# Optimization experiments

Hardware: AMD Instinct MI355X
Metric: run time of the kernel (lower is better)

The kernel has to match this reference:

```python
import math
import jax, jax.numpy as jnp
import numpy as np

N_HEADS = 8
GROUPS = 32
EPS = 1e-5


def setup_inputs() -> dict:
    key = jax.random.key(0)
    ks = jax.random.split(key, 4)
    B, C, H, W = 8, 512, 32, 32
    x = jax.random.normal(ks[0], (B, C, H, W), dtype=jnp.float32)
    gn_scale = jnp.ones((C,), dtype=jnp.float32)
    gn_bias = jnp.zeros((C,), dtype=jnp.float32)
    # small init so softmax logits stay in a sane range (original zero-inits
    # proj_out; we use small random weights so the output is non-trivial)
    qkv_w = jax.random.normal(ks[1], (3 * C, C), dtype=jnp.float32) * 0.02
    qkv_b = jnp.zeros((3 * C,), dtype=jnp.float32)
    proj_w = jax.random.normal(ks[2], (C, C), dtype=jnp.float32) * 0.02
    proj_b = jnp.zeros((C,), dtype=jnp.float32)
    return {"x": x, "gn_scale": gn_scale, "gn_bias": gn_bias,
            "qkv_w": qkv_w, "qkv_b": qkv_b,
            "proj_w": proj_w, "proj_b": proj_b}


def reference(x, gn_scale, gn_bias, qkv_w, qkv_b, proj_w, proj_b):
    b, c, H, W = x.shape
    L = H * W
    xr = x.reshape(b, c, L)

    # GroupNorm32: normalize in fp32 over (channels_per_group, L)
    xf = xr.astype(jnp.float32).reshape(b, GROUPS, -1)
    mu = xf.mean(axis=-1, keepdims=True)
    var = xf.var(axis=-1, keepdims=True)
    xn = ((xf - mu) * jax.lax.rsqrt(var + EPS)).reshape(b, c, L)
    xn = (xn * gn_scale[:, None] + gn_bias[:, None]).astype(x.dtype)

    # 1x1 conv QKV projection: [b, 3C, L]
    qkv = jnp.einsum('oc,bcl->bol', qkv_w, xn) + qkv_b[:, None]

    # QKVAttentionLegacy: split 3C axis as (heads, 3*ch)
    ch = c // N_HEADS
    qkv = qkv.reshape(b * N_HEADS, 3 * ch, L)
    q, k, v = qkv[:, :ch], qkv[:, ch:2 * ch], qkv[:, 2 * ch:]
    scale = 1.0 / math.sqrt(math.sqrt(ch))
    w = jnp.einsum('bct,bcs->bts', q * scale, k * scale)  # [b*h, L, L]
    w = jax.nn.softmax(w.astype(jnp.float32), axis=-1).astype(qkv.dtype)
    a = jnp.einsum('bts,bcs->bct', w, v).reshape(b, c, L)

    # 1x1 conv output projection + residual
    h = jnp.einsum('oc,bcl->bol', proj_w, a) + proj_b[:, None]
    return (xr + h).reshape(b, c, H, W)
```

## Files before the change

### kernel.cpp

```cpp
#include <hip/hip_runtime.h>
#include <hip/hip_bf16.h>

typedef __attribute__((ext_vector_type(8))) short v8s;
typedef __attribute__((ext_vector_type(4))) short v4s;
typedef __attribute__((ext_vector_type(8))) unsigned short u16x8;
typedef __attribute__((ext_vector_type(4))) float v4f;

#define MFMA16(a, b, c) __builtin_amdgcn_mfma_f32_16x16x32_bf16((a), (b), (c), 0, 0, 0)

#if __has_builtin(__builtin_amdgcn_mfma_f32_16x16x16_bf16)
#define MFMA16K16(a, b, c) __builtin_amdgcn_mfma_f32_16x16x16_bf16((a), (b), (c), 0, 0, 0)
#elif __has_builtin(__builtin_amdgcn_mfma_f32_16x16x16bf16_1k)
#define MFMA16K16(a, b, c) __builtin_amdgcn_mfma_f32_16x16x16bf16_1k((a), (b), (c), 0, 0, 0)
#else
static __device__ __forceinline__ v4f mfma16k16_asm(v4s a, v4s b, v4f c) {
  v4f d;
  asm("v_mfma_f32_16x16x16_bf16 %0, %1, %2, %3" : "=v"(d) : "v"(a), "v"(b), "v"(c));
  return d;
}
#define MFMA16K16(a, b, c) mfma16k16_asm((a), (b), (c))
#endif

#define GLL16(g, l)                                                        \
  __builtin_amdgcn_global_load_lds(                                        \
      (const __attribute__((address_space(1))) unsigned int*)(g),          \
      (__attribute__((address_space(3))) unsigned int*)(l), 16, 0, 0)

#if __has_builtin(__builtin_amdgcn_exp2f)
__device__ __forceinline__ float exp2n(float x) { return __builtin_amdgcn_exp2f(x); }
#else
__device__ __forceinline__ float exp2n(float x) {
  float r; asm("v_exp_f32 %0, %1" : "=v"(r) : "v"(x)); return r;
}
#endif

__device__ __forceinline__ unsigned short f2bf(float f) {
  union { float f; unsigned u; } v; v.f = f;
  unsigned r = v.u + 0x7fffu + ((v.u >> 16) & 1u);
  return (unsigned short)(r >> 16);
}
__device__ __forceinline__ unsigned packbf2(float lo, float hi) {
  union { float f; unsigned u; } a, b; a.f = lo; b.f = hi;
  return (a.u >> 16) | (b.u & 0xffff0000u);
}

__global__ __launch_bounds__(256) void cvt_gn_kernel(const float* __restrict__ in0,
                                                     unsigned short* __restrict__ out0,
                                                     const float* __restrict__ in1,
                                                     unsigned short* __restrict__ out1,
                                                     int n0, int n1,
                                                     const float* __restrict__ x,
                                                     float2* __restrict__ stats) {
  if (blockIdx.x < 1024) {
    int i = blockIdx.x * 256 + threadIdx.x;
    const float* in; unsigned short* out;
    if (i < n0) { in = in0; out = out0; }
    else        { i -= n0; if (i >= n1) return; in = in1; out = out1; }
    float4 v = ((const float4*)in)[i];
    ushort4 o;
    o.x = f2bf(v.x); o.y = f2bf(v.y); o.z = f2bf(v.z); o.w = f2bf(v.w);
    ((ushort4*)out)[i] = o;
    return;
  }
  const int bg = blockIdx.x - 1024;
  const float4* xp4 = (const float4*)(x + (size_t)bg * 16 * 1024);
  float s = 0.f, ss = 0.f;
  for (int i = threadIdx.x; i < 4096; i += 256) {
    float4 v = xp4[i];
    s  += (v.x + v.y) + (v.z + v.w);
    ss += (v.x * v.x + v.y * v.y) + (v.z * v.z + v.w * v.w);
  }
  #pragma unroll
  for (int d = 1; d < 64; d <<= 1) { s += __shfl_xor(s, d); ss += __shfl_xor(ss, d); }
  __shared__ float red[2][4];
  const int w = threadIdx.x >> 6;
  if ((threadIdx.x & 63) == 0) { red[0][w] = s; red[1][w] = ss; }
  __syncthreads();
  if (threadIdx.x == 0) {
    s  = red[0][0] + red[0][1] + red[0][2] + red[0][3];
    ss = red[1][0] + red[1][1] + red[1][2] + red[1][3];
    const float mu  = s * (1.f / 16384.f);
    const float var = ss * (1.f / 16384.f) - mu * mu;
    stats[bg] = make_float2(mu, rsqrtf(var + 1e-5f));
  }
}

__global__ __launch_bounds__(256) void gnt_kernel(const float* __restrict__ x,
                                                  const float2* __restrict__ stats,
                                                  const float* __restrict__ gsc,
                                                  const float* __restrict__ gbi,
                                                  unsigned short* __restrict__ xnT) {
  const int b = blockIdx.z, l0 = blockIdx.x * 64, c0 = blockIdx.y * 64;
  const float* sp = x + (size_t)b * 512 * 1024;
  unsigned short* dp = xnT + (size_t)b * 1024 * 512;
  __shared__ unsigned T[64][65];
  const int tid = threadIdx.x;
  const int rr = tid >> 3, c8 = (tid & 7) * 8;
  #pragma unroll
  for (int sw = 0; sw < 2; ++sw) {
    const int c = c0 + sw * 32 + rr;
    const float2 st = stats[b * 32 + (c >> 4)];
    const float sc = gsc[c] * st.y;
    const float bi = gbi[c] - st.x * sc;
    const float4* px = (const float4*)(sp + (size_t)c * 1024 + l0 + c8);
    float4 v0 = px[0], v1 = px[1];
    T[sw * 32 + rr][c8 + 0] = f2bf(v0.x * sc + bi);
    T[sw * 32 + rr][c8 + 1] = f2bf(v0.y * sc + bi);
    T[sw * 32 + rr][c8 + 2] = f2bf(v0.z * sc + bi);
    T[sw * 32 + rr][c8 + 3] = f2bf(v0.w * sc + bi);
    T[sw * 32 + rr][c8 + 4] = f2bf(v1.x * sc + bi);
    T[sw * 32 + rr][c8 + 5] = f2bf(v1.y * sc + bi);
    T[sw * 32 + rr][c8 + 6] = f2bf(v1.z * sc + bi);
    T[sw * 32 + rr][c8 + 7] = f2bf(v1.w * sc + bi);
  }
  __syncthreads();
  #pragma unroll
  for (int sw = 0; sw < 2; ++sw) {
    const int ll = sw * 32 + rr;
    u16x8 o;
    #pragma unroll
    for (int j = 0; j < 8; ++j) o[j] = (unsigned short)T[c8 + j][ll];
    *(u16x8*)(dp + (size_t)(l0 + ll) * 512 + c0 + c8) = o;
  }
}

template <bool QKV, int NT>
__global__ __launch_bounds__(256) void gemm_kernel(
    const unsigned short* __restrict__ A,
    const unsigned short* __restrict__ BT,
    const float* __restrict__ bias,
    const float* __restrict__ xres,
    float* __restrict__ outf,
    unsigned short* __restrict__ qT,
    unsigned short* __restrict__ kT,
    unsigned short* __restrict__ vO) {
  constexpr int K = 512;
  constexpr int NFR = NT / 32;
  constexpr int NJOB = 16 + NT / 8;
  const int n0 = blockIdx.x * NT, m0 = blockIdx.y * 128, b = blockIdx.z;
  const unsigned short* Bp = BT + (size_t)b * 1024 * K;

  __shared__ __align__(16) unsigned short As[128][64];
  __shared__ __align__(16) unsigned short Bs[NT][64];

  const int tid = threadIdx.x, lane = tid & 63, w = tid >> 6;
  const int quad = lane >> 4, l15 = lane & 15;
  const int wm = (w >> 1) * 64, wn = (w & 1) * (NT / 2);
  const int srow = lane >> 3;
  const int scol = ((lane & 7) ^ srow) * 8;
  const int ck0 = ((quad ^ (l15 & 7)) * 8);
  const int ck1 = ck0 ^ 32;
  const unsigned short* Asf = &As[0][0];
  const unsigned short* Bsf = &Bs[0][0];

  v4f acc[4][NFR];
  #pragma unroll
  for (int i = 0; i < 4; ++i)
    #pragma unroll
    for (int j = 0; j < NFR; ++j) acc[i][j] = (v4f){0.f, 0.f, 0.f, 0.f};

  for (int kk = 0; kk < K; kk += 64) {
    __syncthreads();
    #pragma unroll
    for (int jj = 0; jj < NJOB / 4; ++jj) {
      const int job = w * (NJOB / 4) + jj;
      if (job < 16) {
        GLL16(A + (size_t)(m0 + job * 8 + srow) * K + kk + scol, &As[job * 8][0]);
      } else {
        const int j2 = job - 16;
        GLL16(Bp + (size_t)(n0 + j2 * 8 + srow) * K + kk + scol, &Bs[j2 * 8][0]);
      }
    }
    __syncthreads();
    #pragma unroll
    for (int h = 0; h < 2; ++h) {
      const int ck = h ? ck1 : ck0;
      v8s af[4], bf[NFR];
      #pragma unroll
      for (int mt = 0; mt < 4; ++mt) af[mt] = *(const v8s*)(Asf + (wm + mt * 16 + l15) * 64 + ck);
      #pragma unroll
      for (int nt = 0; nt < NFR; ++nt) bf[nt] = *(const v8s*)(Bsf + (wn + nt * 16 + l15) * 64 + ck);
      #pragma unroll
      for (int mt = 0; mt < 4; ++mt)
        #pragma unroll
        for (int nt = 0; nt < NFR; ++nt)
          acc[mt][nt] = MFMA16(af[mt], bf[nt], acc[mt][nt]);
    }
  }

  if (QKV) {
    const int bh8 = b * 8;
    const float cs = 0.18033688011112042f;
    #pragma unroll
    for (int mt = 0; mt < 4; ++mt) {
      const int m4 = m0 + wm + mt * 16 + quad * 4;
      const int h = m4 / 192;
      const int rr = m4 - h * 192;
      const int part = rr >> 6;
      const int ch = rr & 63;
      const float b0 = bias[m4], b1 = bias[m4 + 1], b2 = bias[m4 + 2], b3 = bias[m4 + 3];
      #pragma unroll
      for (int nt = 0; nt < NFR; ++nt) {
        const int n = n0 + wn + nt * 16 + l15;
        v4f a = acc[mt][nt];
        const float v0 = a[0] + b0, v1 = a[1] + b1, v2 = a[2] + b2, v3 = a[3] + b3;
        if (part == 0) {
          ushort4 st4;
          st4.x = f2bf(v0 * cs); st4.y = f2bf(v1 * cs);
          st4.z = f2bf(v2 * cs); st4.w = f2bf(v3 * cs);
          *(ushort4*)(qT + ((size_t)(bh8 + h) * 1024 + n) * 64 + ch) = st4;
        } else if (part == 1) {
          ushort4 st4;
          st4.x = f2bf(v0); st4.y = f2bf(v1); st4.z = f2bf(v2); st4.w = f2bf(v3);
          *(ushort4*)(kT + ((size_t)(bh8 + h) * 1024 + n) * 64 + ch) = st4;
        } else {
          unsigned short* dp = vO + ((size_t)(bh8 + h) * 64 + ch) * 1024 + n;
          dp[0] = f2bf(v0); dp[1024] = f2bf(v1); dp[2048] = f2bf(v2); dp[3072] = f2bf(v3);
        }
      }
    }
  } else {
    #pragma unroll
    for (int mt = 0; mt < 4; ++mt) {
      const int m4 = m0 + wm + mt * 16 + quad * 4;
      const float b0 = bias[m4], b1 = bias[m4 + 1], b2 = bias[m4 + 2], b3 = bias[m4 + 3];
      #pragma unroll
      for (int nt = 0; nt < NFR; ++nt) {
        const int n = n0 + wn + nt * 16 + l15;
        const size_t i0 = ((size_t)b * 512 + m4) * 1024 + n;
        outf[i0]        = xres[i0]        + acc[mt][nt][0] + b0;
        outf[i0 + 1024] = xres[i0 + 1024] + acc[mt][nt][1] + b1;
        outf[i0 + 2048] = xres[i0 + 2048] + acc[mt][nt][2] + b2;
        outf[i0 + 3072] = xres[i0 + 3072] + acc[mt][nt][3] + b3;
      }
    }
  }
}

__global__ __launch_bounds__(256) void attn_kernel(const unsigned short* __restrict__ qT,
                                                   const unsigned short* __restrict__ kT,
                                                   const unsigned short* __restrict__ vv,
                                                   unsigned short* __restrict__ aT) {
  const int bh = blockIdx.x;
  const int t0 = blockIdx.y * 256;
  const unsigned short* qb = qT + (size_t)bh * 1024 * 64;
  const unsigned short* kb = kT + (size_t)bh * 1024 * 64;
  const unsigned short* vb = vv + (size_t)bh * 64 * 1024;

  __shared__ __align__(16) unsigned short Ks[2][128][64];
  __shared__ __align__(16) unsigned short Vs[2][2][64][64];

  const int tid = threadIdx.x, w = tid >> 6, lane = tid & 63;
  const int quad = lane >> 4, l15 = lane & 15;
  const int srow = lane >> 3;
  const int scol = ((lane & 7) ^ srow) * 8;
  const int ck0 = ((quad ^ (l15 & 7)) * 8);
  const int ck1 = ck0 ^ 32;

  #pragma unroll
  for (int jj = 0; jj < 8; ++jj) {
    const int seg = w * 8 + jj;
    GLL16(qb + (size_t)(t0 + seg * 8 + srow) * 64 + scol, &Ks[0][0][0] + seg * 8 * 64);
  }
  __syncthreads();
  v8s qf[4][2];
  #pragma unroll
  for (int tg = 0; tg < 4; ++tg) {
    const int row = w * 64 + tg * 16 + l15;
    qf[tg][0] = *(const v8s*)(&Ks[0][0][0] + row * 64 + ck0);
    qf[tg][1] = *(const v8s*)(&Ks[0][0][0] + row * 64 + ck1);
  }
  __syncthreads();

  #pragma unroll
  for (int jj = 0; jj < 8; ++jj) {
    const int j = w * 8 + jj;
    if (j < 16) {
      GLL16(kb + (size_t)(j * 8 + srow) * 64 + scol, &Ks[0][j * 8][0]);
    } else {
      const int j2 = j - 16, hf = j2 >> 3, cg = (j2 & 7) * 8;
      GLL16(vb + (size_t)(cg + srow) * 1024 + hf * 64 + scol, &Vs[0][hf][cg][0]);
    }
  }

  v4f o[4][4];
  #pragma unroll
  for (int tg = 0; tg < 4; ++tg)
    #pragma unroll
    for (int i = 0; i < 4; ++i) o[tg][i] = (v4f){0.f, 0.f, 0.f, 0.f};
  float lsum[4] = {0.f, 0.f, 0.f, 0.f};

  const int vq4 = (quad & 1) * 4;
  const int vqh = quad >> 1;

  for (int it = 0; it < 8; ++it) {
    __syncthreads();
    if (it + 1 < 8) {
      const int s1 = (it + 1) * 128, bp1 = (it + 1) & 1;
      #pragma unroll
      for (int jj = 0; jj < 8; ++jj) {
        const int j = w * 8 + jj;
        if (j < 16) {
          GLL16(kb + (size_t)(s1 + j * 8 + srow) * 64 + scol, &Ks[bp1][j * 8][0]);
        } else {
          const int j2 = j - 16, hf = j2 >> 3, cg = (j2 & 7) * 8;
          GLL16(vb + (size_t)(cg + srow) * 1024 + s1 + hf * 64 + scol,
                &Vs[bp1][hf][cg][0]);
        }
      }
    }
    const int buf = it & 1;

    #pragma unroll
    for (int hf = 0; hf < 2; ++hf) {
      const unsigned short* Kb = &Ks[buf][hf * 64][0];
      const unsigned short* Vb = &Vs[buf][hf][0][0];

      v8s kf[4][2];
      #pragma unroll
      for (int st = 0; st < 4; ++st) {
        kf[st][0] = *(const v8s*)(Kb + (st * 16 + l15) * 64 + ck0);
        kf[st][1] = *(const v8s*)(Kb + (st * 16 + l15) * 64 + ck1);
      }
      v4s vfr[4][4];
      #pragma unroll
      for (int nc = 0; nc < 4; ++nc) {
        const int row = nc * 16 + l15;
        const unsigned short* vrow = Vb + row * 64 + vq4;
        const int rx = row & 7;
        #pragma unroll
        for (int st = 0; st < 4; ++st)
          vfr[nc][st] = *(const v4s*)(vrow + ((st * 2 + vqh) ^ rx) * 8);
      }

      #pragma unroll
      for (int tg = 0; tg < 4; ++tg) {
        v4f sa[4];
        #pragma unroll
        for (int st = 0; st < 4; ++st) {
          v4f z = (v4f){0.f, 0.f, 0.f, 0.f};
          z = MFMA16(kf[st][0], qf[tg][0], z);
          sa[st] = MFMA16(kf[st][1], qf[tg][1], z);
        }
        union { v4s v; unsigned u[2]; } pa[4];
        float rsum = 0.f;
        #pragma unroll
        for (int st = 0; st < 4; ++st) {
          float p0 = exp2n(sa[st][0]);
          float p1 = exp2n(sa[st][1]);
          float p2 = exp2n(sa[st][2]);
          float p3 = exp2n(sa[st][3]);
          rsum += (p0 + p1) + (p2 + p3);
          pa[st].u[0] = packbf2(p0, p1);
          pa[st].u[1] = packbf2(p2, p3);
        }
        lsum[tg] += rsum;
        #pragma unroll
        for (int nc = 0; nc < 4; ++nc)
          #pragma unroll
          for (int st = 0; st < 4; ++st)
            o[tg][nc] = MFMA16K16(pa[st].v, vfr[nc][st], o[tg][nc]);
      }
    }
  }

  const int b = bh >> 3, h = bh & 7;
  #pragma unroll
  for (int tg = 0; tg < 4; ++tg) {
    lsum[tg] += __shfl_xor(lsum[tg], 16);
    lsum[tg] += __shfl_xor(lsum[tg], 32);
  }
  #pragma unroll
  for (int tg = 0; tg < 4; ++tg) {
    float rl[4];
    #pragma unroll
    for (int r = 0; r < 4; ++r) rl[r] = 1.0f / __shfl(lsum[tg], quad * 4 + r);
    #pragma unroll
    for (int nc = 0; nc < 4; ++nc)
      #pragma unroll
      for (int r = 0; r < 4; ++r) {
        aT[((size_t)b * 1024 + t0 + w * 64 + tg * 16 + quad * 4 + r) * 512 +
           h * 64 + nc * 16 + l15] = f2bf(o[tg][nc][r] * rl[r]);
      }
  }
}

extern "C" void kernel_launch(void* const* d_in, const int* in_sizes, int n_in,
                              void* d_out, int out_size, void* d_ws, size_t ws_size,
                              hipStream_t stream) {
  const float* x    = (const float*)d_in[0];
  const float* gsc  = (const float*)d_in[1];
  const float* gbi  = (const float*)d_in[2];
  const float* qkvw = (const float*)d_in[3];
  const float* qkvb = (const float*)d_in[4];
  const float* pjw  = (const float*)d_in[5];
  const float* pjb  = (const float*)d_in[6];
  float* out = (float*)d_out;

  unsigned short* ws  = (unsigned short*)d_ws;
  unsigned short* qw  = ws;
  unsigned short* pw  = qw + 786432;
  float2* stats = (float2*)(pw + 262144);
  unsigned short* xnT = pw + 262144 + 1024;
  unsigned short* qT  = xnT + 4194304;
  unsigned short* kT  = qT + 4194304;
  unsigned short* vv  = kT + 4194304;
  unsigned short* aT  = vv + 4194304;

  cvt_gn_kernel<<<dim3(1280), dim3(256), 0, stream>>>(qkvw, qw, pjw, pw, 196608, 65536,
                                                      x, stats);
  gnt_kernel<<<dim3(16, 8, 8), dim3(256), 0, stream>>>(x, stats, gsc, gbi, xnT);
  gemm_kernel<true, 128><<<dim3(8, 12, 8), dim3(256), 0, stream>>>(
      qw, xnT, qkvb, nullptr, nullptr, qT, kT, vv);
  attn_kernel<<<dim3(64, 4), dim3(256), 0, stream>>>(qT, kT, vv, aT);
  gemm_kernel<false, 64><<<dim3(16, 4, 8), dim3(256), 0, stream>>>(
      pw, aT, pjb, x, out, nullptr, nullptr, nullptr);
}
```

Measured before the change: 149.4 us.

## Switch attention kernel to 32x32x16 MFMA with permlane-based P repacking

Rewrites the attention inner loop to use 32x32x16 bf16 MFMA tiles for both QK^T and PV instead of 16x16 tiles. The softmax probabilities are packed with v_cvt_pk_bf16_f32 and rearranged between lane halves using v_permlane32_swap so they can feed the PV MFMA directly. This is meant to cut MFMA issue count and LDS fragment loads per flop. In exchange it uses larger accumulators, which raises register pressure, and it relies on gfx950-specific instructions. The packing also changes rounding of P from truncation to the hardware conversion.

```diff
diff --git a/kernel.cpp b/kernel.cpp
--- a/kernel.cpp
+++ b/kernel.cpp
@@ -2,24 +2,12 @@
 #include <hip/hip_bf16.h>
 
 typedef __attribute__((ext_vector_type(8))) short v8s;
-typedef __attribute__((ext_vector_type(4))) short v4s;
 typedef __attribute__((ext_vector_type(8))) unsigned short u16x8;
 typedef __attribute__((ext_vector_type(4))) float v4f;
+typedef __attribute__((ext_vector_type(16))) float f32x16;
 
 #define MFMA16(a, b, c) __builtin_amdgcn_mfma_f32_16x16x32_bf16((a), (b), (c), 0, 0, 0)
-
-#if __has_builtin(__builtin_amdgcn_mfma_f32_16x16x16_bf16)
-#define MFMA16K16(a, b, c) __builtin_amdgcn_mfma_f32_16x16x16_bf16((a), (b), (c), 0, 0, 0)
-#elif __has_builtin(__builtin_amdgcn_mfma_f32_16x16x16bf16_1k)
-#define MFMA16K16(a, b, c) __builtin_amdgcn_mfma_f32_16x16x16bf16_1k((a), (b), (c), 0, 0, 0)
-#else
-static __device__ __forceinline__ v4f mfma16k16_asm(v4s a, v4s b, v4f c) {
-  v4f d;
-  asm("v_mfma_f32_16x16x16_bf16 %0, %1, %2, %3" : "=v"(d) : "v"(a), "v"(b), "v"(c));
-  return d;
-}
-#define MFMA16K16(a, b, c) mfma16k16_asm((a), (b), (c))
-#endif
+#define MFMA32(a, b, c) __builtin_amdgcn_mfma_f32_32x32x16_bf16((a), (b), (c), 0, 0, 0)
 
 #define GLL16(g, l)                                                        \
   __builtin_amdgcn_global_load_lds(                                        \
@@ -39,9 +27,14 @@
   unsigned r = v.u + 0x7fffu + ((v.u >> 16) & 1u);
   return (unsigned short)(r >> 16);
 }
-__device__ __forceinline__ unsigned packbf2(float lo, float hi) {
-  union { float f; unsigned u; } a, b; a.f = lo; b.f = hi;
-  return (a.u >> 16) | (b.u & 0xffff0000u);
+
+__device__ __forceinline__ unsigned cvtpk(float lo, float hi) {
+  unsigned r;
+  asm("v_cvt_pk_bf16_f32 %0, %1, %2" : "=v"(r) : "v"(lo), "v"(hi));
+  return r;
+}
+__device__ __forceinline__ void pl32swap(unsigned& a, unsigned& b) {
+  asm("v_permlane32_swap_b32 %0, %1" : "+v"(a), "+v"(b));
 }
 
 __global__ __launch_bounds__(256) void cvt_gn_kernel(const float* __restrict__ in0,
@@ -251,11 +244,9 @@
   __shared__ __align__(16) unsigned short Vs[2][2][64][64];
 
   const int tid = threadIdx.x, w = tid >> 6, lane = tid & 63;
-  const int quad = lane >> 4, l15 = lane & 15;
+  const int l31 = lane & 31, h = lane >> 5;
   const int srow = lane >> 3;
   const int scol = ((lane & 7) ^ srow) * 8;
-  const int ck0 = ((quad ^ (l15 & 7)) * 8);
-  const int ck1 = ck0 ^ 32;
 
   #pragma unroll
   for (int jj = 0; jj < 8; ++jj) {
@@ -263,12 +254,15 @@
     GLL16(qb + (size_t)(t0 + seg * 8 + srow) * 64 + scol, &Ks[0][0][0] + seg * 8 * 64);
   }
   __syncthreads();
-  v8s qf[4][2];
-  #pragma unroll
-  for (int tg = 0; tg < 4; ++tg) {
-    const int row = w * 64 + tg * 16 + l15;
-    qf[tg][0] = *(const v8s*)(&Ks[0][0][0] + row * 64 + ck0);
-    qf[tg][1] = *(const v8s*)(&Ks[0][0][0] + row * 64 + ck1);
+  v8s qf[2][4];
+  #pragma unroll
+  for (int tb = 0; tb < 2; ++tb) {
+    const int row = w * 64 + tb * 32 + l31;
+    const unsigned short* qr = &Ks[0][0][0] + row * 64;
+    const int rx = row & 7;
+    #pragma unroll
+    for (int kb2 = 0; kb2 < 4; ++kb2)
+      qf[tb][kb2] = *(const v8s*)(qr + ((kb2 * 2 + h) ^ rx) * 8);
   }
   __syncthreads();
 
@@ -283,15 +277,14 @@
     }
   }
 
-  v4f o[4][4];
-  #pragma unroll
-  for (int tg = 0; tg < 4; ++tg)
-    #pragma unroll
-    for (int i = 0; i < 4; ++i) o[tg][i] = (v4f){0.f, 0.f, 0.f, 0.f};
-  float lsum[4] = {0.f, 0.f, 0.f, 0.f};
-
-  const int vq4 = (quad & 1) * 4;
-  const int vqh = quad >> 1;
+  f32x16 o[2][2];
+  #pragma unroll
+  for (int tb = 0; tb < 2; ++tb)
+    #pragma unroll
+    for (int cb = 0; cb < 2; ++cb)
+      #pragma unroll
+      for (int r = 0; r < 16; ++r) o[tb][cb][r] = 0.f;
+  float lsum[2] = {0.f, 0.f};
 
   for (int it = 0; it < 8; ++it) {
     __syncthreads();
@@ -316,72 +309,68 @@
       const unsigned short* Kb = &Ks[buf][hf * 64][0];
       const unsigned short* Vb = &Vs[buf][hf][0][0];
 
-      v8s kf[4][2];
-      #pragma unroll
-      for (int st = 0; st < 4; ++st) {
-        kf[st][0] = *(const v8s*)(Kb + (st * 16 + l15) * 64 + ck0);
-        kf[st][1] = *(const v8s*)(Kb + (st * 16 + l15) * 64 + ck1);
-      }
-      v4s vfr[4][4];
-      #pragma unroll
-      for (int nc = 0; nc < 4; ++nc) {
-        const int row = nc * 16 + l15;
-        const unsigned short* vrow = Vb + row * 64 + vq4;
-        const int rx = row & 7;
+      v8s kf[2][4], vf[2][4];
+      #pragma unroll
+      for (int sb = 0; sb < 2; ++sb) {
+        const int row = sb * 32 + l31, rx = row & 7;
+        const unsigned short* kr = Kb + row * 64;
         #pragma unroll
-        for (int st = 0; st < 4; ++st)
-          vfr[nc][st] = *(const v4s*)(vrow + ((st * 2 + vqh) ^ rx) * 8);
-      }
-
-      #pragma unroll
-      for (int tg = 0; tg < 4; ++tg) {
-        v4f sa[4];
+        for (int kb2 = 0; kb2 < 4; ++kb2)
+          kf[sb][kb2] = *(const v8s*)(kr + ((kb2 * 2 + h) ^ rx) * 8);
+      }
+      #pragma unroll
+      for (int cb = 0; cb < 2; ++cb) {
+        const int row = cb * 32 + l31, rx = row & 7;
+        const unsigned short* vr = Vb + row * 64;
         #pragma unroll
-        for (int st = 0; st < 4; ++st) {
-          v4f z = (v4f){0.f, 0.f, 0.f, 0.f};
-          z = MFMA16(kf[st][0], qf[tg][0], z);
-          sa[st] = MFMA16(kf[st][1], qf[tg][1], z);
+        for (int i = 0; i < 4; ++i)
+          vf[cb][i] = *(const v8s*)(vr + ((i * 2 + h) ^ rx) * 8);
+      }
+
+      #pragma unroll
+      for (int tb = 0; tb < 2; ++tb) {
+        #pragma unroll
+        for (int sb = 0; sb < 2; ++sb) {
+          f32x16 sa = {0.f,0.f,0.f,0.f,0.f,0.f,0.f,0.f,0.f,0.f,0.f,0.f,0.f,0.f,0.f,0.f};
+          #pragma unroll
+          for (int kb2 = 0; kb2 < 4; ++kb2)
+            sa = MFMA32(kf[sb][kb2], qf[tb][kb2], sa);
+          float p[16]; float rsum = 0.f;
+          #pragma unroll
+          for (int r = 0; r < 16; ++r) { p[r] = exp2n(sa[r]); rsum += p[r]; }
+          lsum[tb] += rsum;
+          unsigned c0 = cvtpk(p[0], p[1]),  c1 = cvtpk(p[2], p[3]);
+          unsigned c2 = cvtpk(p[4], p[5]),  c3 = cvtpk(p[6], p[7]);
+          pl32swap(c0, c2); pl32swap(c1, c3);
+          unsigned c4 = cvtpk(p[8], p[9]),  c5 = cvtpk(p[10], p[11]);
+          unsigned c6 = cvtpk(p[12], p[13]), c7 = cvtpk(p[14], p[15]);
+          pl32swap(c4, c6); pl32swap(c5, c7);
+          union { v8s v; unsigned u[4]; } pa0, pa1;
+          pa0.u[0] = c0; pa0.u[1] = c1; pa0.u[2] = c2; pa0.u[3] = c3;
+          pa1.u[0] = c4; pa1.u[1] = c5; pa1.u[2] = c6; pa1.u[3] = c7;
+          #pragma unroll
+          for (int cb = 0; cb < 2; ++cb) {
+            o[tb][cb] = MFMA32(pa0.v, vf[cb][sb * 2 + 0], o[tb][cb]);
+            o[tb][cb] = MFMA32(pa1.v, vf[cb][sb * 2 + 1], o[tb][cb]);
+          }
         }
-        union { v4s v; unsigned u[2]; } pa[4];
-        float rsum = 0.f;
-        #pragma unroll
-        for (int st = 0; st < 4; ++st) {
-          float p0 = exp2n(sa[st][0]);
-          float p1 = exp2n(sa[st][1]);
-          float p2 = exp2n(sa[st][2]);
-          float p3 = exp2n(sa[st][3]);
-          rsum += (p0 + p1) + (p2 + p3);
-          pa[st].u[0] = packbf2(p0, p1);
-          pa[st].u[1] = packbf2(p2, p3);
-        }
-        lsum[tg] += rsum;
-        #pragma unroll
-        for (int nc = 0; nc < 4; ++nc)
-          #pragma unroll
-          for (int st = 0; st < 4; ++st)
-            o[tg][nc] = MFMA16K16(pa[st].v, vfr[nc][st], o[tg][nc]);
-      }
-    }
-  }
-
-  const int b = bh >> 3, h = bh & 7;
-  #pragma unroll
-  for (int tg = 0; tg < 4; ++tg) {
-    lsum[tg] += __shfl_xor(lsum[tg], 16);
-    lsum[tg] += __shfl_xor(lsum[tg], 32);
-  }
-  #pragma unroll
-  for (int tg = 0; tg < 4; ++tg) {
-    float rl[4];
-    #pragma unroll
-    for (int r = 0; r < 4; ++r) rl[r] = 1.0f / __shfl(lsum[tg], quad * 4 + r);
-    #pragma unroll
-    for (int nc = 0; nc < 4; ++nc)
-      #pragma unroll
-      for (int r = 0; r < 4; ++r) {
-        aT[((size_t)b * 1024 + t0 + w * 64 + tg * 16 + quad * 4 + r) * 512 +
-           h * 64 + nc * 16 + l15] = f2bf(o[tg][nc][r] * rl[r]);
-      }
+      }
+    }
+  }
+
+  const int b = bh >> 3, hd = bh & 7;
+  #pragma unroll
+  for (int tb = 0; tb < 2; ++tb) {
+    lsum[tb] += __shfl_xor(lsum[tb], 32);
+    #pragma unroll
+    for (int r = 0; r < 16; ++r) {
+      const int trow = (r & 3) + 8 * (r >> 2) + 4 * h;
+      const float inv = 1.0f / __shfl(lsum[tb], trow);
+      const int t = t0 + w * 64 + tb * 32 + trow;
+      unsigned short* dst = aT + ((size_t)b * 1024 + t) * 512 + hd * 64;
+      dst[l31]      = f2bf(o[tb][0][r] * inv);
+      dst[32 + l31] = f2bf(o[tb][1][r] * inv);
+    }
   }
 }
 
```

New measurement: 148.6 us. About the same (-0.5%).
